# Performance work log

Measured on AMD Instinct MI355X. Metric: run time of the kernel, lower is better.

The kernel has to match this reference:

```python
import jax, jax.numpy as jnp
import numpy as np

STATIC_TH = 0.05
TRIM_RATIO = 0.2
EPS = 1e-6


def setup_inputs() -> dict:
    key = jax.random.key(0)
    k1, k2, k3 = jax.random.split(key, 3)
    B, T, H, W = 2, 32, 518, 518
    pred_disp = jax.random.uniform(k1, (B, T, H, W), jnp.float32, 0.01, 10.0)
    gt_depth = jax.random.uniform(k2, (B, T, H, W), jnp.float32, 0.1, 80.0)
    mask = jax.random.uniform(k3, (B, T, H, W)) > 0.2
    return {"pred_disp": pred_disp, "gt_depth": gt_depth, "mask": mask}


def _nanquantile_rows(vals, valid, q):
    """torch.nanquantile(dim=1, interpolation='linear') where invalid entries are NaN.
    vals: [N,Q] float, valid: [N,Q] bool. Returns [N] threshold (NaN if row empty)."""
    big = jnp.where(valid, vals, jnp.inf)          # invalid -> +inf, sorts to the end
    srt = jnp.sort(big, axis=1)                    # [N,Q]
    nv = valid.sum(axis=1)                         # valid count per row
    pos = q * jnp.maximum(nv - 1, 0).astype(vals.dtype)
    lo = jnp.floor(pos).astype(jnp.int32)
    hi = jnp.ceil(pos).astype(jnp.int32)
    frac = pos - lo.astype(vals.dtype)
    vlo = jnp.take_along_axis(srt, lo[:, None], axis=1)[:, 0]
    vhi = jnp.take_along_axis(srt, hi[:, None], axis=1)[:, 0]
    thresh = vlo * (1.0 - frac) + vhi * frac
    return jnp.where(nv > 0, thresh, jnp.nan)      # empty row -> NaN (keep-mask all False)


def reference(pred_disp, gt_depth, mask):
    B, T, H, W = pred_disp.shape
    raw = jnp.clip(pred_disp, EPS)                 # [B,T,H,W]
    gt_disp = 1.0 / jnp.clip(gt_depth, EPS)

    # per-batch least-squares scale/shift alignment on masked pixels
    raw_f = raw.reshape(B, -1)
    gt_f = gt_disp.reshape(B, -1)
    mf = mask.reshape(B, -1).astype(raw.dtype)
    count = jnp.maximum(mf.sum(axis=1, keepdims=True), 1.0)
    mean_raw = (raw_f * mf).sum(axis=1, keepdims=True) / count
    mean_gt = (gt_f * mf).sum(axis=1, keepdims=True) / count
    d_c = (raw_f - mean_raw) * mf
    g_c = (gt_f - mean_gt) * mf
    cov = (d_c * g_c).sum(axis=1, keepdims=True)
    var = jnp.maximum((d_c * d_c).sum(axis=1, keepdims=True), EPS)
    s = cov / var
    t = mean_gt - s * mean_raw
    aligned = (raw_f * s + t).reshape(B, T, H, W)

    # temporal gradient matching on static pixels
    d_diff = jnp.abs(aligned[:, 1:] - aligned[:, :-1])     # [B,T-1,H,W]
    g_diff = jnp.abs(gt_disp[:, 1:] - gt_disp[:, :-1])
    valid_pair = mask[:, 1:] & mask[:, :-1]
    depth_diff = jnp.abs(gt_depth[:, 1:] - gt_depth[:, :-1])
    static = valid_pair & (depth_diff < STATIC_TH)
    err = jnp.abs(d_diff - g_diff)

    N = B * (T - 1)
    Q = H * W
    err2 = err.reshape(N, Q)
    st2 = static.reshape(N, Q)

    # trimmed (robust) masked mean per frame pair
    thresh = _nanquantile_rows(err2, st2, 1.0 - TRIM_RATIO)   # [N]
    keep = st2 & (err2 <= thresh[:, None])
    sum_err = (err2 * keep.astype(err2.dtype)).sum(axis=1)
    cnt = jnp.maximum(keep.sum(axis=1).astype(err2.dtype), 1.0)
    loss_frame = sum_err / cnt
    return loss_frame.mean()
```

## Files before the change

kernel.cpp:

```cpp
#include <hip/hip_runtime.h>
#include <math.h>

#define HW      268324
#define HW4     67081
#define T_      32
#define B_      2
#define NPAIR   31
#define NROW    62
#define GX      263
#define NBLKB   (2*GX)
#define NF      17
#define CAP     2048
#define CSTR    16
#define EPSF    1e-6f
#define STH     0.05f

typedef float fx4 __attribute__((ext_vector_type(4)));
typedef int   ix4 __attribute__((ext_vector_type(4)));


__device__ __forceinline__ float fast_rcp(float x) {
    float r = __builtin_amdgcn_rcpf(x);
    float e = fmaf(-x, r, 1.0f);
    return fmaf(r, e, r);
}

__device__ __forceinline__ fx4 nt_load4(const float* p) {
    return __builtin_nontemporal_load((const fx4*)p);
}
__device__ __forceinline__ ix4 nt_load4i(const int* p) {
    return __builtin_nontemporal_load((const ix4*)p);
}
__device__ __forceinline__ unsigned int nt_loadu(const unsigned char* p) {
    return __builtin_nontemporal_load((const unsigned int*)p);
}

__device__ __forceinline__ int word_bad(unsigned int w) {
    return (w != 0u && w != 1u && w != 0xFFFFFFFFu && w != 0x3F800000u) ? 1 : 0;
}

__global__ void init_detect_kernel(const unsigned int* __restrict__ m,
                                   int* __restrict__ flag,
                                   int* __restrict__ cnt,
                                   float* __restrict__ out) {
    const int tid = threadIdx.x;
    for (int i = tid; i < NROW * CSTR; i += 256) cnt[i] = 0;
    if (tid == 0) out[0] = 0.0f;

    const unsigned int* mm = m;
    int bad = 0;
    #pragma unroll
    for (int u = 0; u < 16; ++u) {
        const unsigned int w = mm[u * 256 + tid];
        bad |= word_bad(w);
    }
    #pragma unroll
    for (int o = 32; o > 0; o >>= 1) bad |= __shfl_down(bad, o);
    __shared__ int red[4];
    const int wid = tid >> 6, lane = tid & 63;
    if (lane == 0) red[wid] = bad;
    __syncthreads();
    if (tid == 0) *flag = (red[0] | red[1] | red[2] | red[3]) ? 1 : 0;
}

__launch_bounds__(256)
__global__ void pass1_kernel(const float* __restrict__ pred,
                             const float* __restrict__ depth,
                             const void*  __restrict__ maskp,
                             const int*   __restrict__ flag,
                             double* __restrict__ partials,
                             int*    __restrict__ cnt,
                             float*  __restrict__ rbuf,
                             float*  __restrict__ gbuf)
{
    const int byteFmt = *flag;
    const int p4 = blockIdx.x * 256 + threadIdx.x;
    const bool active = (p4 < HW4);
    const int p4c = active ? p4 : (HW4 - 1);
    const int b = blockIdx.y >> 1;
    const int h = blockIdx.y & 1;
    const int fs = h * 15;
    const size_t base = (size_t)b * T_ * HW + (size_t)fs * HW + (size_t)p4c * 4;

    const float* pp = pred + base;
    const float* dd = depth + base;
    const unsigned char* m8 = (const unsigned char*)maskp + base;
    const int* m32 = (const int*)maskp + base;

    fx4 pvs[3], dvs[3];
    unsigned int mws[3];
    ix4 mis[3];

    #pragma unroll
    for (int k = 0; k < 2; ++k) {
        pvs[k] = nt_load4(pp + (size_t)k * HW);
        dvs[k] = nt_load4(dd + (size_t)k * HW);
        if (byteFmt) mws[k] = nt_loadu(m8 + (size_t)k * HW);
        else         mis[k] = nt_load4i(m32 + (size_t)k * HW);
    }

    int scn = 0;
    float f_r = 0.f, f_g = 0.f, f_rg = 0.f, f_rr = 0.f;
    float pcr[4], pcg[4], pcd[4];
    unsigned int pmb = 0u;

    #pragma unroll
    for (int k = 0; k < NF; ++k) {
        if (k + 2 < NF) {
            const int s2 = (k + 2) % 3;
            pvs[s2] = nt_load4(pp + (size_t)(k + 2) * HW);
            dvs[s2] = nt_load4(dd + (size_t)(k + 2) * HW);
            if (byteFmt) mws[s2] = nt_loadu(m8 + (size_t)(k + 2) * HW);
            else         mis[s2] = nt_load4i(m32 + (size_t)(k + 2) * HW);
        }
        const int s = k % 3;
        unsigned int mb;
        if (byteFmt) {
            const unsigned int w = mws[s];
            mb = ((w & 0x000000FFu) ? 1u : 0u) | ((w & 0x0000FF00u) ? 2u : 0u)
               | ((w & 0x00FF0000u) ? 4u : 0u) | ((w & 0xFF000000u) ? 8u : 0u);
        } else {
            const ix4 mi = mis[s];
            mb = (mi.x ? 1u : 0u) | (mi.y ? 2u : 0u) | (mi.z ? 4u : 0u) | (mi.w ? 8u : 0u);
        }
        if (!active) mb = 0u;

        const float px[4] = {pvs[s].x, pvs[s].y, pvs[s].z, pvs[s].w};
        const float dx[4] = {dvs[s].x, dvs[s].y, dvs[s].z, dvs[s].w};
        float cr[4], cg[4], cd[4];
        #pragma unroll
        for (int j = 0; j < 4; ++j) {
            cr[j] = fmaxf(px[j], EPSF);
            cd[j] = dx[j];
            cg[j] = fast_rcp(fmaxf(dx[j], EPSF));
        }

        if (k >= h && k < 16 + h) {
            #pragma unroll
            for (int j = 0; j < 4; ++j) {
                const bool m = (mb >> j) & 1u;
                const float rm = m ? cr[j] : 0.0f;
                const float gm = m ? cg[j] : 0.0f;
                scn += m ? 1 : 0;
                f_r += rm; f_g += gm;
                f_rg = fmaf(rm, gm, f_rg);
                f_rr = fmaf(rm, rm, f_rr);
            }
        }

        if (k >= 1 && (h == 1 || k <= 15)) {
            const int row = b * NPAIR + fs + k - 1;
            #pragma unroll
            for (int j = 0; j < 4; ++j) {
                if (((mb >> j) & (pmb >> j) & 1u) && fabsf(cd[j] - pcd[j]) < STH) {
                    const int pos = atomicAdd(&cnt[row * CSTR], 1);
                    if (pos < CAP) {
                        rbuf[row * CAP + pos] = fabsf(cr[j] - pcr[j]);
                        gbuf[row * CAP + pos] = fabsf(cg[j] - pcg[j]);
                    }
                }
            }
        }

        #pragma unroll
        for (int j = 0; j < 4; ++j) { pcr[j] = cr[j]; pcg[j] = cg[j]; pcd[j] = cd[j]; }
        pmb = mb;
    }

    double v1 = (double)f_r, v2 = (double)f_g, v3 = (double)f_rg, v4 = (double)f_rr;
    int vc = scn;
    #pragma unroll
    for (int o = 32; o > 0; o >>= 1) {
        v1 += __shfl_down(v1, o); v2 += __shfl_down(v2, o);
        v3 += __shfl_down(v3, o); v4 += __shfl_down(v4, o);
        vc += __shfl_down(vc, o);
    }
    __shared__ double red[4][4];
    __shared__ int redc[4];
    const int wid = threadIdx.x >> 6, lane = threadIdx.x & 63;
    if (lane == 0) { red[wid][0]=v1; red[wid][1]=v2; red[wid][2]=v3; red[wid][3]=v4; redc[wid]=vc; }
    __syncthreads();
    if (threadIdx.x == 0) {
        double* p = partials + (size_t)(blockIdx.y * GX + blockIdx.x) * 5;
        p[0] = (double)(redc[0] + redc[1] + redc[2] + redc[3]);
        p[1] = red[0][0]+red[1][0]+red[2][0]+red[3][0];
        p[2] = red[0][1]+red[1][1]+red[2][1]+red[3][1];
        p[3] = red[0][2]+red[1][2]+red[2][2]+red[3][2];
        p[4] = red[0][3]+red[1][3]+red[2][3]+red[3][3];
    }
}

__launch_bounds__(256)
__global__ void rowquant_kernel(const double* __restrict__ partials,
                                const int* __restrict__ cnt,
                                const float* __restrict__ rbuf,
                                const float* __restrict__ gbuf,
                                float* __restrict__ out)
{
    __shared__ float arr[CAP];
    __shared__ double rs[4][5];
    __shared__ float s_sa;
    __shared__ int   s_P;
    const int row = blockIdx.x;
    const int bb  = row / NPAIR;
    const int wid = threadIdx.x >> 6, lane = threadIdx.x & 63;

    const double* p = partials + (size_t)bb * NBLKB * 5;
    double v[5] = {0, 0, 0, 0, 0};
    for (int i = threadIdx.x; i < NBLKB; i += 256) {
        #pragma unroll
        for (int j = 0; j < 5; ++j) v[j] += p[i * 5 + j];
    }
    #pragma unroll
    for (int o = 32; o > 0; o >>= 1) {
        #pragma unroll
        for (int j = 0; j < 5; ++j) v[j] += __shfl_down(v[j], o);
    }
    if (lane == 0) {
        #pragma unroll
        for (int j = 0; j < 5; ++j) rs[wid][j] = v[j];
    }
    __syncthreads();

    int n = cnt[row * CSTR]; if (n > CAP) n = CAP;
    if (threadIdx.x == 0) {
        const double c0  = rs[0][0]+rs[1][0]+rs[2][0]+rs[3][0];
        const double sr  = rs[0][1]+rs[1][1]+rs[2][1]+rs[3][1];
        const double sg  = rs[0][2]+rs[1][2]+rs[2][2]+rs[3][2];
        const double srg = rs[0][3]+rs[1][3]+rs[2][3]+rs[3][3];
        const double srr = rs[0][4]+rs[1][4]+rs[2][4]+rs[3][4];
        const double count = fmax(c0, 1.0);
        const double mr = sr / count, mg = sg / count;
        const double cov = srg - mr * sg - mg * sr + c0 * mr * mg;
        double       var = srr - 2.0 * mr * sr + c0 * mr * mr;
        var = fmax(var, 1e-6);
        s_sa = (float)fabs(cov / var);
        int P = 64; while (P < n) P <<= 1;
        s_P = P;
    }
    __syncthreads();
    const float sa = s_sa;
    const int   P  = s_P;

    for (int i = threadIdx.x; i < P; i += 256) {
        float e = INFINITY;
        if (i < n) e = fabsf(sa * rbuf[row * CAP + i] - gbuf[row * CAP + i]);
        arr[i] = e;
    }
    __syncthreads();

    for (int k = 2; k <= P; k <<= 1) {
        for (int j = k >> 1; j > 0; j >>= 1) {
            for (int i = threadIdx.x; i < P; i += 256) {
                const int ij = i ^ j;
                if (ij > i) {
                    const float a = arr[i], bv = arr[ij];
                    const bool up = ((i & k) == 0);
                    if ((a > bv) == up) { arr[i] = bv; arr[ij] = a; }
                }
            }
            __syncthreads();
        }
    }

    __shared__ float sthresh;
    if (threadIdx.x == 0) {
        if (n > 0) {
            const float pos  = 0.8f * (float)(n - 1);
            const int   lo   = (int)floorf(pos);
            const int   hi   = (int)ceilf(pos);
            const float frac = pos - (float)lo;
            sthresh = arr[lo] * (1.0f - frac) + arr[hi] * frac;
        } else {
            sthresh = -1.0f;
        }
    }
    __syncthreads();
    const float th = sthresh;

    double lsum = 0.0; int lcnt = 0;
    for (int i = threadIdx.x; i < n; i += 256) {
        const float e = arr[i];
        if (e <= th) { lsum += (double)e; lcnt++; }
    }
    #pragma unroll
    for (int o = 32; o > 0; o >>= 1) { lsum += __shfl_down(lsum, o); lcnt += __shfl_down(lcnt, o); }
    __shared__ double rr[4]; __shared__ int rc[4];
    if (lane == 0) { rr[wid] = lsum; rc[wid] = lcnt; }
    __syncthreads();
    if (threadIdx.x == 0) {
        const double tot = rr[0] + rr[1] + rr[2] + rr[3];
        const int    tc  = rc[0] + rc[1] + rc[2] + rc[3];
        const double loss_row = tot / (double)(tc > 0 ? tc : 1);
        atomicAdd(out, (float)(loss_row * (1.0 / (double)NROW)));
    }
}

extern "C" void kernel_launch(void* const* d_in, const int* in_sizes, int n_in,
                              void* d_out, int out_size, void* d_ws, size_t ws_size,
                              hipStream_t stream) {
    const float* pred  = (const float*)d_in[0];
    const float* depth = (const float*)d_in[1];
    const void*  mask  = d_in[2];
    float* out = (float*)d_out;

    char* ws = (char*)d_ws;
    int*    flag       = (int*)(ws + 0);
    int*    cnt        = (int*)(ws + 64);
    double* partials   = (double*)(ws + 8192);
    float*  rbuf       = (float*)(ws + 180224);
    float*  gbuf       = (float*)(ws + 688128);

    init_detect_kernel<<<1, 256, 0, stream>>>((const unsigned int*)mask, flag, cnt, out);
    dim3 g1(GX, B_ * 2);
    pass1_kernel<<<g1, 256, 0, stream>>>(pred, depth, mask, flag, partials, cnt, rbuf, gbuf);
    rowquant_kernel<<<NROW, 256, 0, stream>>>(partials, cnt, rbuf, gbuf, out);
}
```

Before: 211.8 us.

## Process all 32 frames per block and deepen load prefetch to five slots

Each block now walks all 32 frames of a batch instead of splitting the time axis into two halves, so the one overlapping frame no longer has to be loaded twice. The grid halves to GX x B blocks. The software prefetch ring grows from 3 to 5 slots to keep more loads in flight per thread. The trade-off is half as many blocks, which means fewer waves to hide latency, plus higher register pressure from the larger ring.

```diff
diff --git a/kernel.cpp b/kernel.cpp
--- a/kernel.cpp
+++ b/kernel.cpp
@@ -8,8 +8,9 @@
 #define NPAIR   31
 #define NROW    62
 #define GX      263
-#define NBLKB   (2*GX)
-#define NF      17
+#define NBLKB   GX
+#define NF      32
+#define SLOTS   5
 #define CAP     2048
 #define CSTR    16
 #define EPSF    1e-6f
@@ -77,22 +78,20 @@
     const int p4 = blockIdx.x * 256 + threadIdx.x;
     const bool active = (p4 < HW4);
     const int p4c = active ? p4 : (HW4 - 1);
-    const int b = blockIdx.y >> 1;
-    const int h = blockIdx.y & 1;
-    const int fs = h * 15;
-    const size_t base = (size_t)b * T_ * HW + (size_t)fs * HW + (size_t)p4c * 4;
+    const int b = blockIdx.y;
+    const size_t base = (size_t)b * T_ * HW + (size_t)p4c * 4;
 
     const float* pp = pred + base;
     const float* dd = depth + base;
     const unsigned char* m8 = (const unsigned char*)maskp + base;
     const int* m32 = (const int*)maskp + base;
 
-    fx4 pvs[3], dvs[3];
-    unsigned int mws[3];
-    ix4 mis[3];
-
-    #pragma unroll
-    for (int k = 0; k < 2; ++k) {
+    fx4 pvs[SLOTS], dvs[SLOTS];
+    unsigned int mws[SLOTS];
+    ix4 mis[SLOTS];
+
+    #pragma unroll
+    for (int k = 0; k < SLOTS - 1; ++k) {
         pvs[k] = nt_load4(pp + (size_t)k * HW);
         dvs[k] = nt_load4(dd + (size_t)k * HW);
         if (byteFmt) mws[k] = nt_loadu(m8 + (size_t)k * HW);
@@ -106,14 +105,14 @@
 
     #pragma unroll
     for (int k = 0; k < NF; ++k) {
-        if (k + 2 < NF) {
-            const int s2 = (k + 2) % 3;
-            pvs[s2] = nt_load4(pp + (size_t)(k + 2) * HW);
-            dvs[s2] = nt_load4(dd + (size_t)(k + 2) * HW);
-            if (byteFmt) mws[s2] = nt_loadu(m8 + (size_t)(k + 2) * HW);
-            else         mis[s2] = nt_load4i(m32 + (size_t)(k + 2) * HW);
-        }
-        const int s = k % 3;
+        if (k + SLOTS - 1 < NF) {
+            const int s2 = (k + SLOTS - 1) % SLOTS;
+            pvs[s2] = nt_load4(pp + (size_t)(k + SLOTS - 1) * HW);
+            dvs[s2] = nt_load4(dd + (size_t)(k + SLOTS - 1) * HW);
+            if (byteFmt) mws[s2] = nt_loadu(m8 + (size_t)(k + SLOTS - 1) * HW);
+            else         mis[s2] = nt_load4i(m32 + (size_t)(k + SLOTS - 1) * HW);
+        }
+        const int s = k % SLOTS;
         unsigned int mb;
         if (byteFmt) {
             const unsigned int w = mws[s];
@@ -135,21 +134,19 @@
             cg[j] = fast_rcp(fmaxf(dx[j], EPSF));
         }
 
-        if (k >= h && k < 16 + h) {
-            #pragma unroll
-            for (int j = 0; j < 4; ++j) {
-                const bool m = (mb >> j) & 1u;
-                const float rm = m ? cr[j] : 0.0f;
-                const float gm = m ? cg[j] : 0.0f;
-                scn += m ? 1 : 0;
-                f_r += rm; f_g += gm;
-                f_rg = fmaf(rm, gm, f_rg);
-                f_rr = fmaf(rm, rm, f_rr);
-            }
-        }
-
-        if (k >= 1 && (h == 1 || k <= 15)) {
-            const int row = b * NPAIR + fs + k - 1;
+        #pragma unroll
+        for (int j = 0; j < 4; ++j) {
+            const bool m = (mb >> j) & 1u;
+            const float rm = m ? cr[j] : 0.0f;
+            const float gm = m ? cg[j] : 0.0f;
+            scn += m ? 1 : 0;
+            f_r += rm; f_g += gm;
+            f_rg = fmaf(rm, gm, f_rg);
+            f_rr = fmaf(rm, rm, f_rr);
+        }
+
+        if (k >= 1) {
+            const int row = b * NPAIR + k - 1;
             #pragma unroll
             for (int j = 0; j < 4; ++j) {
                 if (((mb >> j) & (pmb >> j) & 1u) && fabsf(cd[j] - pcd[j]) < STH) {
@@ -312,7 +309,7 @@
     float*  gbuf       = (float*)(ws + 688128);
 
     init_detect_kernel<<<1, 256, 0, stream>>>((const unsigned int*)mask, flag, cnt, out);
-    dim3 g1(GX, B_ * 2);
+    dim3 g1(GX, B_);
     pass1_kernel<<<g1, 256, 0, stream>>>(pred, depth, mask, flag, partials, cnt, rbuf, gbuf);
     rowquant_kernel<<<NROW, 256, 0, stream>>>(partials, cnt, rbuf, gbuf, out);
 }
```

New measurement: 223.3 us. +5.4%, slower.

## Fuse pass1 and row-quantile kernels with last-block ticket and host mask-format detection

Applied to the files above, without the earlier changes.

Replaces the three-kernel sequence with one templated kernel. The mask format is decided on the host from the input sizes instead of a detection kernel, and counters are cleared with hipMemsetAsync. The final NROW blocks to take a ticket spin-wait until every block has finished, then compute the per-row quantile and trimmed mean. This removes launch gaps and the flag load, but adds a spin-wait and a ticket counter that depends on those blocks being co-resident.

```diff
diff --git a/kernel.cpp b/kernel.cpp
--- a/kernel.cpp
+++ b/kernel.cpp
@@ -8,8 +8,11 @@
 #define NPAIR   31
 #define NROW    62
 #define GX      263
+#define NYB     4
+#define TOTALB  (GX*NYB)
 #define NBLKB   (2*GX)
 #define NF      17
+#define SLOTS   3
 #define CAP     2048
 #define CSTR    16
 #define EPSF    1e-6f
@@ -35,45 +38,17 @@
     return __builtin_nontemporal_load((const unsigned int*)p);
 }
 
-__device__ __forceinline__ int word_bad(unsigned int w) {
-    return (w != 0u && w != 1u && w != 0xFFFFFFFFu && w != 0x3F800000u) ? 1 : 0;
-}
-
-__global__ void init_detect_kernel(const unsigned int* __restrict__ m,
-                                   int* __restrict__ flag,
-                                   int* __restrict__ cnt,
-                                   float* __restrict__ out) {
-    const int tid = threadIdx.x;
-    for (int i = tid; i < NROW * CSTR; i += 256) cnt[i] = 0;
-    if (tid == 0) out[0] = 0.0f;
-
-    const unsigned int* mm = m;
-    int bad = 0;
-    #pragma unroll
-    for (int u = 0; u < 16; ++u) {
-        const unsigned int w = mm[u * 256 + tid];
-        bad |= word_bad(w);
-    }
-    #pragma unroll
-    for (int o = 32; o > 0; o >>= 1) bad |= __shfl_down(bad, o);
-    __shared__ int red[4];
-    const int wid = tid >> 6, lane = tid & 63;
-    if (lane == 0) red[wid] = bad;
-    __syncthreads();
-    if (tid == 0) *flag = (red[0] | red[1] | red[2] | red[3]) ? 1 : 0;
-}
-
-__launch_bounds__(256)
-__global__ void pass1_kernel(const float* __restrict__ pred,
+template<int BYTEFMT>
+__global__ void fused_kernel(const float* __restrict__ pred,
                              const float* __restrict__ depth,
                              const void*  __restrict__ maskp,
-                             const int*   __restrict__ flag,
                              double* __restrict__ partials,
                              int*    __restrict__ cnt,
                              float*  __restrict__ rbuf,
-                             float*  __restrict__ gbuf)
+                             float*  __restrict__ gbuf,
+                             int*    __restrict__ done,
+                             float*  __restrict__ out)
 {
-    const int byteFmt = *flag;
     const int p4 = blockIdx.x * 256 + threadIdx.x;
     const bool active = (p4 < HW4);
     const int p4c = active ? p4 : (HW4 - 1);
@@ -87,15 +62,15 @@
     const unsigned char* m8 = (const unsigned char*)maskp + base;
     const int* m32 = (const int*)maskp + base;
 
-    fx4 pvs[3], dvs[3];
-    unsigned int mws[3];
-    ix4 mis[3];
-
-    #pragma unroll
-    for (int k = 0; k < 2; ++k) {
+    fx4 pvs[SLOTS], dvs[SLOTS];
+    unsigned int mws[SLOTS];
+    ix4 mis[SLOTS];
+
+    #pragma unroll
+    for (int k = 0; k < SLOTS - 1; ++k) {
         pvs[k] = nt_load4(pp + (size_t)k * HW);
         dvs[k] = nt_load4(dd + (size_t)k * HW);
-        if (byteFmt) mws[k] = nt_loadu(m8 + (size_t)k * HW);
+        if (BYTEFMT) mws[k] = nt_loadu(m8 + (size_t)k * HW);
         else         mis[k] = nt_load4i(m32 + (size_t)k * HW);
     }
 
@@ -107,15 +82,15 @@
     #pragma unroll
     for (int k = 0; k < NF; ++k) {
         if (k + 2 < NF) {
-            const int s2 = (k + 2) % 3;
+            const int s2 = (k + 2) % SLOTS;
             pvs[s2] = nt_load4(pp + (size_t)(k + 2) * HW);
             dvs[s2] = nt_load4(dd + (size_t)(k + 2) * HW);
-            if (byteFmt) mws[s2] = nt_loadu(m8 + (size_t)(k + 2) * HW);
+            if (BYTEFMT) mws[s2] = nt_loadu(m8 + (size_t)(k + 2) * HW);
             else         mis[s2] = nt_load4i(m32 + (size_t)(k + 2) * HW);
         }
-        const int s = k % 3;
+        const int s = k % SLOTS;
         unsigned int mb;
-        if (byteFmt) {
+        if (BYTEFMT) {
             const unsigned int w = mws[s];
             mb = ((w & 0x000000FFu) ? 1u : 0u) | ((w & 0x0000FF00u) ? 2u : 0u)
                | ((w & 0x00FF0000u) ? 4u : 0u) | ((w & 0xFF000000u) ? 8u : 0u);
@@ -188,22 +163,27 @@
         p[3] = red[0][2]+red[1][2]+red[2][2]+red[3][2];
         p[4] = red[0][3]+red[1][3]+red[2][3]+red[3][3];
     }
-}
-
-__launch_bounds__(256)
-__global__ void rowquant_kernel(const double* __restrict__ partials,
-                                const int* __restrict__ cnt,
-                                const float* __restrict__ rbuf,
-                                const float* __restrict__ gbuf,
-                                float* __restrict__ out)
-{
+
+    __threadfence();
+    __syncthreads();
+    __shared__ int s_ticket;
+    if (threadIdx.x == 0) s_ticket = atomicAdd(done, 1);
+    __syncthreads();
+    const int ticket = s_ticket;
+    if (ticket < TOTALB - NROW) return;
+    const int row = ticket - (TOTALB - NROW);
+
+    if (threadIdx.x == 0) {
+        while (__hip_atomic_load(done, __ATOMIC_ACQUIRE, __HIP_MEMORY_SCOPE_AGENT) < TOTALB)
+            __builtin_amdgcn_s_sleep(2);
+    }
+    __syncthreads();
+
     __shared__ float arr[CAP];
     __shared__ double rs[4][5];
     __shared__ float s_sa;
     __shared__ int   s_P;
-    const int row = blockIdx.x;
-    const int bb  = row / NPAIR;
-    const int wid = threadIdx.x >> 6, lane = threadIdx.x & 63;
+    const int bb = row / NPAIR;
 
     const double* p = partials + (size_t)bb * NBLKB * 5;
     double v[5] = {0, 0, 0, 0, 0};
@@ -285,12 +265,12 @@
     }
     #pragma unroll
     for (int o = 32; o > 0; o >>= 1) { lsum += __shfl_down(lsum, o); lcnt += __shfl_down(lcnt, o); }
-    __shared__ double rr[4]; __shared__ int rc[4];
-    if (lane == 0) { rr[wid] = lsum; rc[wid] = lcnt; }
-    __syncthreads();
-    if (threadIdx.x == 0) {
-        const double tot = rr[0] + rr[1] + rr[2] + rr[3];
-        const int    tc  = rc[0] + rc[1] + rc[2] + rc[3];
+    __shared__ double rr2[4]; __shared__ int rc2[4];
+    if (lane == 0) { rr2[wid] = lsum; rc2[wid] = lcnt; }
+    __syncthreads();
+    if (threadIdx.x == 0) {
+        const double tot = rr2[0] + rr2[1] + rr2[2] + rr2[3];
+        const int    tc  = rc2[0] + rc2[1] + rc2[2] + rc2[3];
         const double loss_row = tot / (double)(tc > 0 ? tc : 1);
         atomicAdd(out, (float)(loss_row * (1.0 / (double)NROW)));
     }
@@ -305,14 +285,20 @@
     float* out = (float*)d_out;
 
     char* ws = (char*)d_ws;
-    int*    flag       = (int*)(ws + 0);
     int*    cnt        = (int*)(ws + 64);
+    int*    done       = (int*)(ws + 4032);
     double* partials   = (double*)(ws + 8192);
     float*  rbuf       = (float*)(ws + 180224);
     float*  gbuf       = (float*)(ws + 688128);
 
-    init_detect_kernel<<<1, 256, 0, stream>>>((const unsigned int*)mask, flag, cnt, out);
-    dim3 g1(GX, B_ * 2);
-    pass1_kernel<<<g1, 256, 0, stream>>>(pred, depth, mask, flag, partials, cnt, rbuf, gbuf);
-    rowquant_kernel<<<NROW, 256, 0, stream>>>(partials, cnt, rbuf, gbuf, out);
-}
+    const int byteFmt = (in_sizes[2] != in_sizes[0]) ? 1 : 0;
+
+    hipMemsetAsync(ws + 64, 0, 4032, stream);
+    hipMemsetAsync(out, 0, sizeof(float), stream);
+
+    dim3 g1(GX, NYB);
+    if (byteFmt)
+        fused_kernel<1><<<g1, 256, 0, stream>>>(pred, depth, mask, partials, cnt, rbuf, gbuf, done, out);
+    else
+        fused_kernel<0><<<g1, 256, 0, stream>>>(pred, depth, mask, partials, cnt, rbuf, gbuf, done, out);
+}
```

Measured after the change: 372.3 us. 75.8% more time.
